# Kernel tuning notes

Hardware: AMD Instinct MI355X
Metric: run time of the kernel (lower is better)

The kernel has to match this reference:

```python
import jax, jax.numpy as jnp
import numpy as np

B, S, D, H = 2, 2048, 1024, 16
HD = D // H                      # 64
NUM_ROPE_DIMS = 2
NF = HD // (2 * NUM_ROPE_DIMS)   # 16 freqs per rope dim -> total HD//2
FFN_H = 4 * D


def householder_matrix(vs):
    """Product of Householder reflections: Q = prod_i (I - 2 v_i v_i^T / ||v_i||^2)."""
    dim = vs.shape[-1]
    def step(Q, v):
        v = v[:, None]
        Q = Q - (2.0 / (jnp.sum(v * v) + 1e-8)) * (v @ (v.T @ Q))
        return Q, None
    Q, _ = jax.lax.scan(step, jnp.eye(dim, dtype=vs.dtype), vs)
    return Q


def rmsnorm(x):
    # torch.nn.RMSNorm(eps=None) uses dtype eps, no affine
    return x * jax.lax.rsqrt(jnp.mean(x * x, axis=-1, keepdims=True) + jnp.finfo(x.dtype).eps)


def setup_inputs() -> dict:
    key = jax.random.key(0)
    ks = jax.random.split(key, 8)
    x = jax.random.normal(ks[0], (B, S, D), jnp.float32)
    mask = jnp.tril(jnp.ones((S, S), dtype=bool))          # causal block mask
    qkv_w = jax.random.normal(ks[1], (3 * D, D), jnp.float32) * 0.02
    out_w = jax.random.normal(ks[2], (D, D), jnp.float32) * 0.02
    gate_w = jax.random.normal(ks[3], (D, D), jnp.float32) * 0.02
    gate_b = jnp.zeros((D,), jnp.float32)
    w12 = jax.random.normal(ks[4], (2 * FFN_H, D), jnp.float32) * 0.02
    w3 = jax.random.normal(ks[5], (D, FFN_H), jnp.float32) * 0.02
    hh_vs = jax.random.normal(ks[6], (HD // 2, HD), jnp.float32) * 0.02
    inv_freq = 1.0 / (10000.0 ** (jnp.arange(NF, dtype=jnp.float32) / NF))
    pos = jnp.arange(S, dtype=jnp.float32)
    rope_pos = jnp.stack([pos, pos], axis=-1)              # [S, num_rope_dims]
    return dict(x=x, mask=mask, qkv_w=qkv_w, out_w=out_w, gate_w=gate_w,
                gate_b=gate_b, w12=w12, w3=w3, hh_vs=hh_vs,
                inv_freq=inv_freq, rope_pos=rope_pos)


def reference(x, mask, qkv_w, out_w, gate_w, gate_b, w12, w3, hh_vs, inv_freq, rope_pos):
    Bs, Ss, Ds = x.shape
    resid = x
    xn = rmsnorm(x)
    qkv = xn @ qkv_w.T                                      # [B,S,3D]
    q, k, v = jnp.split(qkv, 3, axis=-1)
    q = q.reshape(Bs, Ss, H, HD).transpose(0, 2, 1, 3)      # [B,H,S,HD]
    k = k.reshape(Bs, Ss, H, HD).transpose(0, 2, 1, 3)
    v = v.reshape(Bs, Ss, H, HD).transpose(0, 2, 1, 3)

    # RnRoPE: rotate into canonical basis, apply RoPE, rotate back
    Q = householder_matrix(hh_vs)                           # [HD,HD]
    q = q @ Q.T
    k = k @ Q.T
    # geo_state.scale = 1.0
    full = jnp.einsum('sd,f->sdf', rope_pos, inv_freq).reshape(Ss, -1)  # [S, HD//2]
    half = HD // 2
    full = full[:, :half]
    emb = jnp.concatenate([full, full], axis=-1)            # [S, HD]
    cos, sin = jnp.cos(emb), jnp.sin(emb)

    def rot(t):
        t1, t2 = jnp.split(t, 2, axis=-1)
        return t * cos + jnp.concatenate([-t2, t1], axis=-1) * sin

    q = rot(q) @ Q
    k = rot(k) @ Q

    # block-masked attention (flex_attention default scale = 1/sqrt(HD))
    scores = jnp.einsum('bhsd,bhtd->bhst', q, k) / jnp.sqrt(jnp.asarray(HD, x.dtype))
    scores = jnp.where(mask, scores, -jnp.inf)
    attn = jax.nn.softmax(scores, axis=-1)
    o = jnp.einsum('bhst,bhtd->bhsd', attn, v)
    o = o.transpose(0, 2, 1, 3).reshape(Bs, Ss, Ds)
    o = o @ out_w.T
    gate = jax.nn.sigmoid(o @ gate_w.T + gate_b)
    x = resid + o * gate

    # SwiGLU FFN
    resid2 = x
    xn2 = rmsnorm(x)
    x12 = xn2 @ w12.T
    x1, x2 = jnp.split(x12, 2, axis=-1)
    ffn = (jax.nn.silu(x1) * x2) @ w3.T
    return resid2 + ffn
```

## Files before the change

kernel.cpp:

```cpp
#include <hip/hip_runtime.h>
#include <hip/hip_bf16.h>
#include <math.h>

constexpr int Bc = 2, Sc = 2048, Dc = 1024, Hc = 16, HDc = 64;
constexpr int D3 = 3 * Dc;

typedef __bf16 bf16x8 __attribute__((ext_vector_type(8)));
typedef float f32x4 __attribute__((ext_vector_type(4)));

__device__ __forceinline__ void gll16(const void* g, void* l) {
  __builtin_amdgcn_global_load_lds((const __attribute__((address_space(1))) unsigned int*)g,
                                   (__attribute__((address_space(3))) unsigned int*)l,
                                   16, 0, 0);
}

__device__ __forceinline__ unsigned short f2bf(float v) {
  __hip_bfloat16 h = __float2bfloat16(v);
  return *(unsigned short*)&h;
}
__device__ __forceinline__ float b2f(unsigned short u) {
  unsigned v = ((unsigned)u) << 16;
  return __uint_as_float(v);
}

__global__ __launch_bounds__(256) void f2b_kernel(const float* __restrict__ in,
                                                  unsigned short* __restrict__ out) {
  int i = blockIdx.x * 256 + threadIdx.x;
  float4 v = ((const float4*)in)[i];
  ushort4 o;
  o.x = f2bf(v.x); o.y = f2bf(v.y); o.z = f2bf(v.z); o.w = f2bf(v.w);
  ((ushort4*)out)[i] = o;
}

__global__ __launch_bounds__(256) void rmsnorm_bf16_kernel(const float* __restrict__ in,
                                                           unsigned short* __restrict__ out) {
  int row = blockIdx.x;
  const float4* x4 = (const float4*)(in + (size_t)row * Dc);
  float4 v = x4[threadIdx.x];
  float s = v.x * v.x + v.y * v.y + v.z * v.z + v.w * v.w;
#pragma unroll
  for (int off = 1; off < 64; off <<= 1) s += __shfl_xor(s, off);
  __shared__ float wsum[4];
  if ((threadIdx.x & 63) == 0) wsum[threadIdx.x >> 6] = s;
  __syncthreads();
  float tot = wsum[0] + wsum[1] + wsum[2] + wsum[3];
  float r = rsqrtf(tot * (1.0f / Dc) + 1.1920928955078125e-07f);
  ushort4 o;
  o.x = f2bf(v.x * r); o.y = f2bf(v.y * r); o.z = f2bf(v.z * r); o.w = f2bf(v.w * r);
  ((ushort4*)(out + (size_t)row * Dc))[threadIdx.x] = o;
}

__global__ __launch_bounds__(64) void hh_kernel(const float* __restrict__ vs,
                                                float* __restrict__ Qout) {
  __shared__ float Qm[64][65];
  __shared__ float vsh[64];
  int t = threadIdx.x;
  for (int i = 0; i < 64; ++i) Qm[i][t] = (i == t) ? 1.0f : 0.0f;
  for (int it = 0; it < 32; ++it) {
    __syncthreads();
    vsh[t] = vs[it * 64 + t];
    __syncthreads();
    float nv = 0.0f;
    for (int i = 0; i < 64; ++i) nv += vsh[i] * vsh[i];
    float c = 2.0f / (nv + 1e-8f);
    float wj = 0.0f;
    for (int i = 0; i < 64; ++i) wj += vsh[i] * Qm[i][t];
    for (int i = 0; i < 64; ++i) Qm[i][t] -= c * vsh[i] * wj;
  }
  __syncthreads();
  for (int i = 0; i < 64; ++i) Qout[i * 64 + t] = Qm[i][t];
}

__global__ __launch_bounds__(256) void wqk_kernel(const float* __restrict__ W,
                                                  const float* __restrict__ Qm,
                                                  unsigned short* __restrict__ out) {
  int n = blockIdx.x;
  int r = n & 63;
  int base = n & ~63;
  int t = threadIdx.x;
  float a0 = 0, a1 = 0, a2 = 0, a3 = 0;
  const float4* Wp = (const float4*)(W + (size_t)base * 1024) + t;
#pragma unroll 8
  for (int e = 0; e < 64; ++e) {
    float q = Qm[r * 64 + e];
    float4 wv = Wp[(size_t)e * 256];
    a0 += q * wv.x; a1 += q * wv.y; a2 += q * wv.z; a3 += q * wv.w;
  }
  float sc = (n < 1024) ? 0.18033688f : 1.0f;
  ushort4 o;
  o.x = f2bf(a0 * sc); o.y = f2bf(a1 * sc); o.z = f2bf(a2 * sc); o.w = f2bf(a3 * sc);
  ((ushort4*)(out + (size_t)n * 1024))[t] = o;
}

__global__ __launch_bounds__(256) void rtab_kernel(const float* __restrict__ rope_pos,
                                                   const float* __restrict__ inv_freq,
                                                   float2* __restrict__ tab) {
  int id = blockIdx.x * 256 + threadIdx.x;
  int s = id >> 5, d = id & 31;
  float pos = rope_pos[s * 2 + (d >> 4)];
  float emb = pos * inv_freq[d & 15];
  tab[id] = make_float2(cosf(emb), sinf(emb));
}

__global__ __launch_bounds__(256) void rope_kernel(const unsigned short* __restrict__ qkv,
                                                   const float2* __restrict__ tab,
                                                   unsigned short* __restrict__ qb,
                                                   unsigned short* __restrict__ kb) {
  int t = threadIdx.x;
  int gid = blockIdx.x * 64 + (t >> 2);
  int sub = t & 3;
  int h = gid & 15;
  int which = (gid >> 4) & 1;
  int tok = gid >> 5;
  int s = tok & (Sc - 1), b = tok >> 11;
  const unsigned short* src = qkv + (size_t)tok * D3 + which * Dc + h * 64 + sub * 8;
  uint4 lov = *(const uint4*)src;
  uint4 hiv = *(const uint4*)(src + 32);
  const unsigned short* lp = (const unsigned short*)&lov;
  const unsigned short* hp = (const unsigned short*)&hiv;
  unsigned short olo[8], ohi[8];
  const float2* tp = tab + s * 32 + sub * 8;
#pragma unroll
  for (int i = 0; i < 8; ++i) {
    float2 cs = tp[i];
    float lo = b2f(lp[i]), hi = b2f(hp[i]);
    olo[i] = f2bf(lo * cs.x - hi * cs.y);
    ohi[i] = f2bf(hi * cs.x + lo * cs.y);
  }
  unsigned short* dst = (which ? kb : qb) + ((size_t)((b * Hc + h) * Sc + s)) * 64 + sub * 8;
  *(uint4*)dst = *(uint4*)olo;
  *(uint4*)(dst + 32) = *(uint4*)ohi;
}

__global__ __launch_bounds__(256) void vt_kernel(const unsigned short* __restrict__ qkv,
                                                 unsigned short* __restrict__ vtb) {
  __shared__ unsigned short tile[64 * 72];
  int st = blockIdx.x;
  int bh = blockIdx.y;
  int b = bh >> 4, h = bh & 15;
  int t = threadIdx.x;
  int srow = t >> 2, c16 = (t & 3) * 16;
  const unsigned short* src =
      qkv + (size_t)(b * Sc + st * 64 + srow) * D3 + 2 * Dc + h * 64 + c16;
  uint4 a0 = *(const uint4*)src;
  uint4 a1 = *(const uint4*)(src + 8);
  *(uint4*)(tile + srow * 72 + c16) = a0;
  *(uint4*)(tile + srow * 72 + c16 + 8) = a1;
  __syncthreads();
  int d = t >> 2, sch = (t & 3) * 16;
  unsigned short tmp[16];
#pragma unroll
  for (int i = 0; i < 16; ++i) tmp[i] = tile[(sch + i) * 72 + d];
  unsigned short* dst = vtb + ((size_t)(bh * 64 + d)) * Sc + st * 64 + sch;
  *(uint4*)dst = *(uint4*)tmp;
  *(uint4*)(dst + 8) = *(uint4*)(tmp + 8);
}

template <int MODE>
__global__ __launch_bounds__(256, 2) void mgemm(const unsigned short* __restrict__ A,
                                                const unsigned short* __restrict__ W,
                                                const unsigned short* __restrict__ W2,
                                                void* __restrict__ Cout,
                                                int M, int N, int K) {
  __shared__ unsigned short As[4096];
  __shared__ unsigned short Bs[4096];
  __shared__ unsigned short B2s[(MODE == 1) ? 4096 : 8];
  const int t = threadIdx.x;
  const int lane = t & 63;
  const int wave = t >> 6;
  const int wr = wave >> 1, wc = wave & 1;
  const int m0 = blockIdx.y * 128, n0 = blockIdx.x * 128;
  f32x4 acc[4][4] = {};
  f32x4 acc2[4][4] = {};
  const int srow = t >> 2;
  const int sch = (t & 3) * 8;
  const unsigned short* Ag = A + (size_t)(m0 + srow) * K + sch;
  const unsigned short* Wg = W + (size_t)(n0 + srow) * K + sch;
  const unsigned short* W2g = (MODE == 1) ? (W2 + (size_t)(n0 + srow) * K + sch) : nullptr;
  const size_t rstep = (size_t)64 * K;
  const int frow = lane & 15;
  const int fk = (lane >> 4) * 8;
  for (int k0 = 0; k0 < K; k0 += 32) {
    __syncthreads();
    gll16(Ag + k0, As + t * 8);
    gll16(Ag + k0 + rstep, As + 2048 + t * 8);
    gll16(Wg + k0, Bs + t * 8);
    gll16(Wg + k0 + rstep, Bs + 2048 + t * 8);
    if (MODE == 1) {
      gll16(W2g + k0, B2s + t * 8);
      gll16(W2g + k0 + rstep, B2s + 2048 + t * 8);
    }
    __syncthreads();
    bf16x8 af[4], bq[4];
#pragma unroll
    for (int i = 0; i < 4; ++i)
      af[i] = *(const bf16x8*)(As + (wr * 64 + i * 16 + frow) * 32 + fk);
#pragma unroll
    for (int j = 0; j < 4; ++j)
      bq[j] = *(const bf16x8*)(Bs + (wc * 64 + j * 16 + frow) * 32 + fk);
#pragma unroll
    for (int i = 0; i < 4; ++i)
#pragma unroll
      for (int j = 0; j < 4; ++j)
        acc[i][j] = __builtin_amdgcn_mfma_f32_16x16x32_bf16(af[i], bq[j], acc[i][j], 0, 0, 0);
    if (MODE == 1) {
#pragma unroll
      for (int j = 0; j < 4; ++j)
        bq[j] = *(const bf16x8*)(B2s + (wc * 64 + j * 16 + frow) * 32 + fk);
#pragma unroll
      for (int i = 0; i < 4; ++i)
#pragma unroll
        for (int j = 0; j < 4; ++j)
          acc2[i][j] = __builtin_amdgcn_mfma_f32_16x16x32_bf16(af[i], bq[j], acc2[i][j], 0, 0, 0);
    }
  }
  const int crow = wr * 64 + (lane >> 4) * 4;
  const int ccol = wc * 64 + (lane & 15);
#pragma unroll
  for (int i = 0; i < 4; ++i) {
#pragma unroll
    for (int j = 0; j < 4; ++j) {
#pragma unroll
      for (int r = 0; r < 4; ++r) {
        int row = m0 + crow + i * 16 + r;
        int col = n0 + ccol + j * 16;
        float v = acc[i][j][r];
        size_t off = (size_t)row * N + col;
        if (MODE == 1) {
          float sv = v / (1.0f + expf(-v));
          ((unsigned short*)Cout)[off] = f2bf(sv * acc2[i][j][r]);
        } else {
          ((unsigned short*)Cout)[off] = f2bf(v);
        }
      }
    }
  }
}

template <int MODE>
__global__ __launch_bounds__(256, 3) void mgemm64(const unsigned short* __restrict__ A,
                                                  const unsigned short* __restrict__ W,
                                                  const float* __restrict__ R,
                                                  const float* __restrict__ R2,
                                                  const float* __restrict__ bias,
                                                  void* __restrict__ Cout,
                                                  void* __restrict__ Cout2,
                                                  int M, int N, int K) {
  __shared__ unsigned short As[2048];
  __shared__ unsigned short Bs[4096];
  const int t = threadIdx.x;
  const int lane = t & 63;
  const int wave = t >> 6;
  const int wr = wave >> 1, wc = wave & 1;
  const int m0 = blockIdx.y * 64, n0 = blockIdx.x * 128;
  f32x4 acc[2][4] = {};
  const int srow = t >> 2;
  const int sch = (t & 3) * 8;
  const unsigned short* Ag = A + (size_t)(m0 + srow) * K + sch;
  const unsigned short* Wg = W + (size_t)(n0 + srow) * K + sch;
  const size_t rstep = (size_t)64 * K;
  const int frow = lane & 15;
  const int fk = (lane >> 4) * 8;
  for (int k0 = 0; k0 < K; k0 += 32) {
    __syncthreads();
    gll16(Ag + k0, As + t * 8);
    gll16(Wg + k0, Bs + t * 8);
    gll16(Wg + k0 + rstep, Bs + 2048 + t * 8);
    __syncthreads();
    bf16x8 af[2], bq[4];
#pragma unroll
    for (int i = 0; i < 2; ++i)
      af[i] = *(const bf16x8*)(As + (wr * 32 + i * 16 + frow) * 32 + fk);
#pragma unroll
    for (int j = 0; j < 4; ++j)
      bq[j] = *(const bf16x8*)(Bs + (wc * 64 + j * 16 + frow) * 32 + fk);
#pragma unroll
    for (int i = 0; i < 2; ++i)
#pragma unroll
      for (int j = 0; j < 4; ++j)
        acc[i][j] = __builtin_amdgcn_mfma_f32_16x16x32_bf16(af[i], bq[j], acc[i][j], 0, 0, 0);
  }
  const int crow = wr * 32 + (lane >> 4) * 4;
  const int ccol = wc * 64 + (lane & 15);
#pragma unroll
  for (int i = 0; i < 2; ++i) {
#pragma unroll
    for (int j = 0; j < 4; ++j) {
#pragma unroll
      for (int r = 0; r < 4; ++r) {
        int row = m0 + crow + i * 16 + r;
        int col = n0 + ccol + j * 16;
        float v = acc[i][j][r];
        size_t off = (size_t)row * N + col;
        if (MODE == 2) {
          ((float*)Cout)[off] = v + R[off];
        } else if (MODE == 4) {
          ((float*)Cout)[off] = v;
          ((unsigned short*)Cout2)[off] = f2bf(v);
        } else {
          float g = v + bias[col];
          float sg = 1.0f / (1.0f + expf(-g));
          ((float*)Cout)[off] = R[off] + R2[off] * sg;
        }
      }
    }
  }
}

__global__ __launch_bounds__(256) void mattn(const unsigned short* __restrict__ qb,
                                             const unsigned short* __restrict__ kb,
                                             const unsigned short* __restrict__ vtb,
                                             unsigned short* __restrict__ out) {
  __shared__ unsigned short Qs[8192];
  __shared__ unsigned short Ks[4096];
  __shared__ unsigned short Vts[4096];
  __shared__ unsigned short Ps[4 * 16 * 72];
  const int qt = gridDim.x - 1 - blockIdx.x;
  const int bh = blockIdx.y;
  const int b = bh >> 4, h = bh & 15;
  const int t = threadIdx.x, lane = t & 63, w = t >> 6;
  const int l15 = lane & 15, l4 = lane >> 4;
  const unsigned short* qbase = qb + ((size_t)bh * Sc + qt * 128) * 64;
  const unsigned short* kbase = kb + (size_t)bh * Sc * 64;
  const unsigned short* vbase = vtb + (size_t)bh * 64 * Sc;
#pragma unroll
  for (int i = 0; i < 4; ++i) {
    int idx = t + i * 256;
    int r = idx >> 3;
    int cg = (idx & 7) ^ (r & 7);
    gll16(qbase + (size_t)r * 64 + cg * 8, Qs + idx * 8);
  }
  bf16x8 qf[2][2];
  f32x4 oacc[2][4] = {};
  float lrow[2][4] = {};
  unsigned short* pw = Ps + w * 16 * 72;
  const int ktmax = 2 * qt + 1;
  for (int kt = 0; kt <= ktmax; ++kt) {
    __syncthreads();
    {
      int r = t >> 3;
      int cg = (t & 7) ^ (r & 7);
      gll16(kbase + (size_t)(kt * 64 + r) * 64 + cg * 8, Ks + t * 8);
      gll16(kbase + (size_t)(kt * 64 + r + 32) * 64 + cg * 8, Ks + 2048 + t * 8);
      gll16(vbase + (size_t)r * Sc + kt * 64 + cg * 8, Vts + t * 8);
      gll16(vbase + (size_t)(r + 32) * Sc + kt * 64 + cg * 8, Vts + 2048 + t * 8);
    }
    __syncthreads();
    if (kt == 0) {
#pragma unroll
      for (int ch = 0; ch < 2; ++ch) {
        int qrow = ch * 64 + w * 16 + l15;
#pragma unroll
        for (int kc = 0; kc < 2; ++kc)
          qf[ch][kc] = *(const bf16x8*)(Qs + qrow * 64 + (((kc * 4 + l4) ^ (l15 & 7)) * 8));
      }
    }
    const bool actA = (kt <= 2 * qt);
    f32x4 sc[2][4] = {};
#pragma unroll
    for (int kc = 0; kc < 2; ++kc) {
      bf16x8 kf[4];
#pragma unroll
      for (int j = 0; j < 4; ++j)
        kf[j] = *(const bf16x8*)(Ks + (j * 16 + l15) * 64 + (((kc * 4 + l4) ^ (l15 & 7)) * 8));
      if (actA) {
#pragma unroll
        for (int j = 0; j < 4; ++j)
          sc[0][j] = __builtin_amdgcn_mfma_f32_16x16x32_bf16(qf[0][kc], kf[j], sc[0][j], 0, 0, 0);
      }
#pragma unroll
      for (int j = 0; j < 4; ++j)
        sc[1][j] = __builtin_amdgcn_mfma_f32_16x16x32_bf16(qf[1][kc], kf[j], sc[1][j], 0, 0, 0);
    }
    const int rl = w * 16 + l4 * 4;
    if (kt == 2 * qt) {
#pragma unroll
      for (int j = 0; j < 4; ++j)
#pragma unroll
        for (int r = 0; r < 4; ++r)
          if (j * 16 + l15 > rl + r) sc[0][j][r] = -INFINITY;
    }
    if (kt == ktmax) {
#pragma unroll
      for (int j = 0; j < 4; ++j)
#pragma unroll
        for (int r = 0; r < 4; ++r)
          if (j * 16 + l15 > rl + r) sc[1][j][r] = -INFINITY;
    }
    bf16x8 vf[2][4];
#pragma unroll
    for (int kc = 0; kc < 2; ++kc)
#pragma unroll
      for (int j = 0; j < 4; ++j)
        vf[kc][j] = *(const bf16x8*)(Vts + (j * 16 + l15) * 64 + (((kc * 4 + l4) ^ (l15 & 7)) * 8));
#pragma unroll
    for (int ch = 0; ch < 2; ++ch) {
      if (ch == 0 && !actA) continue;
#pragma unroll
      for (int j = 0; j < 4; ++j)
#pragma unroll
        for (int r = 0; r < 4; ++r) {
          float p = exp2f(sc[ch][j][r]);
          lrow[ch][r] += p;
          pw[(l4 * 4 + r) * 72 + j * 16 + l15] = f2bf(p);
        }
      __asm__ __volatile__("s_waitcnt lgkmcnt(0)" ::: "memory");
#pragma unroll
      for (int kc = 0; kc < 2; ++kc) {
        bf16x8 pf = *(const bf16x8*)(pw + l15 * 72 + kc * 32 + l4 * 8);
#pragma unroll
        for (int j = 0; j < 4; ++j)
          oacc[ch][j] = __builtin_amdgcn_mfma_f32_16x16x32_bf16(pf, vf[kc][j], oacc[ch][j], 0, 0, 0);
      }
    }
  }
#pragma unroll
  for (int ch = 0; ch < 2; ++ch) {
#pragma unroll
    for (int r = 0; r < 4; ++r) {
      float s = lrow[ch][r];
      s += __shfl_xor(s, 1);
      s += __shfl_xor(s, 2);
      s += __shfl_xor(s, 4);
      s += __shfl_xor(s, 8);
      float inv = 1.0f / s;
#pragma unroll
      for (int j = 0; j < 4; ++j) {
        int srow = qt * 128 + ch * 64 + w * 16 + l4 * 4 + r;
        out[((size_t)(b * Sc + srow)) * Dc + h * 64 + j * 16 + l15] =
            f2bf(oacc[ch][j][r] * inv);
      }
    }
  }
}

extern "C" void kernel_launch(void* const* d_in, const int* in_sizes, int n_in,
                              void* d_out, int out_size, void* d_ws, size_t ws_size,
                              hipStream_t stream) {
  const float* x        = (const float*)d_in[0];
  const float* qkv_w    = (const float*)d_in[2];
  const float* out_w    = (const float*)d_in[3];
  const float* gate_w   = (const float*)d_in[4];
  const float* gate_b   = (const float*)d_in[5];
  const float* w12      = (const float*)d_in[6];
  const float* w3       = (const float*)d_in[7];
  const float* hh_vs    = (const float*)d_in[8];
  const float* inv_freq = (const float*)d_in[9];
  const float* rope_pos = (const float*)d_in[10];
  char* ws = (char*)d_ws;
  unsigned short* woutb  = (unsigned short*)(ws + 0);
  float2*         rtab   = (float2*)(ws + 2097152);
  unsigned short* wqkvb  = (unsigned short*)(ws + 4194304);
  unsigned short* attnb  = (unsigned short*)(ws + 4194304);
  float*          xmid   = (float*)(ws + 0);
  unsigned short* slotB  = (unsigned short*)(ws + 16777216);
  float*          oproj  = (float*)(ws + 25165824);
  unsigned short* w12b   = (unsigned short*)(ws + 25165824);
  unsigned short* wgateb = (unsigned short*)(ws + 41943040);
  unsigned short* w3b    = (unsigned short*)(ws + 41943040);
  unsigned short* qkvb   = (unsigned short*)(ws + 58720256);
  unsigned short* hbufb  = (unsigned short*)(ws + 58720256);
  unsigned short* qb     = (unsigned short*)(ws + 83886080);
  unsigned short* oprojb = (unsigned short*)(ws + 83886080);
  unsigned short* kb     = (unsigned short*)(ws + 92274688);
  unsigned short* vtb    = (unsigned short*)(ws + 100663296);
  float*          Qb     = (float*)(ws + 109051904);
  float* outp = (float*)d_out;

  hh_kernel<<<1, 64, 0, stream>>>(hh_vs, Qb);
  rtab_kernel<<<256, 256, 0, stream>>>(rope_pos, inv_freq, rtab);
  wqk_kernel<<<2048, 256, 0, stream>>>(qkv_w, Qb, wqkvb);
  f2b_kernel<<<1024, 256, 0, stream>>>(qkv_w + 2048 * 1024,
                                       wqkvb + 2048 * 1024);
  f2b_kernel<<<1024, 256, 0, stream>>>(out_w, woutb);
  f2b_kernel<<<1024, 256, 0, stream>>>(gate_w, wgateb);
  rmsnorm_bf16_kernel<<<4096, 256, 0, stream>>>(x, slotB);
  mgemm<3><<<dim3(24, 32), 256, 0, stream>>>(slotB, wqkvb, nullptr, qkvb, 4096, 3072, 1024);
  rope_kernel<<<2048, 256, 0, stream>>>(qkvb, rtab, qb, kb);
  vt_kernel<<<dim3(32, 32), 256, 0, stream>>>(qkvb, vtb);
  mattn<<<dim3(16, 32), 256, 0, stream>>>(qb, kb, vtb, attnb);
  mgemm64<4><<<dim3(8, 64), 256, 0, stream>>>(attnb, woutb, nullptr, nullptr, nullptr,
                                              oproj, oprojb, 4096, 1024, 1024);
  mgemm64<5><<<dim3(8, 64), 256, 0, stream>>>(oprojb, wgateb, x, oproj, gate_b,
                                              xmid, nullptr, 4096, 1024, 1024);
  f2b_kernel<<<8192, 256, 0, stream>>>(w12, w12b);
  f2b_kernel<<<4096, 256, 0, stream>>>(w3, w3b);
  rmsnorm_bf16_kernel<<<4096, 256, 0, stream>>>(xmid, slotB);
  mgemm<1><<<dim3(32, 32), 256, 0, stream>>>(slotB, w12b, w12b + 4194304, hbufb,
                                             4096, 4096, 1024);
  mgemm64<2><<<dim3(8, 64), 256, 0, stream>>>(hbufb, w3b, xmid, nullptr, nullptr,
                                              outp, nullptr, 4096, 1024, 4096);
}
```

Measured before the change: 563.3 us.

## Replace QKV and W12 GEMMs with 256x256 double-buffered 8-wave kernel

Adds a new GEMM kernel with 256x256 tiles, 512 threads and 8 waves. It double-buffers K=64 tiles in 128KB of LDS, interleaves global_load_lds prefetch with MFMA phases under manual barriers and setprio, and remaps block ids with an XCD-style swizzle. The w12 conversion now interleaves gate and up rows in 16-row groups, so a single GEMM computes both halves and fuses SiLU*mul in the epilogue. Larger tiles give more data reuse but allow only one block per CU, which may leave CUs idle on the QKV grid (192 blocks).

```diff
diff --git a/kernel.cpp b/kernel.cpp
--- a/kernel.cpp
+++ b/kernel.cpp
@@ -22,6 +22,8 @@
   unsigned v = ((unsigned)u) << 16;
   return __uint_as_float(v);
 }
+
+#define SBAR() asm volatile("s_barrier" ::: "memory")
 
 __global__ __launch_bounds__(256) void f2b_kernel(const float* __restrict__ in,
                                                   unsigned short* __restrict__ out) {
@@ -30,6 +32,17 @@
   ushort4 o;
   o.x = f2bf(v.x); o.y = f2bf(v.y); o.z = f2bf(v.z); o.w = f2bf(v.w);
   ((ushort4*)out)[i] = o;
+}
+
+__global__ __launch_bounds__(256) void w12i_kernel(const float* __restrict__ in,
+                                                   unsigned short* __restrict__ out) {
+  int r = blockIdx.x;
+  int g = r >> 5, u = r & 31;
+  int src = ((u < 16) ? 0 : 4096) + g * 16 + (u & 15);
+  float4 v = ((const float4*)(in + (size_t)src * 1024))[threadIdx.x];
+  ushort4 o;
+  o.x = f2bf(v.x); o.y = f2bf(v.y); o.z = f2bf(v.z); o.w = f2bf(v.w);
+  ((ushort4*)(out + (size_t)r * 1024))[threadIdx.x] = o;
 }
 
 __global__ __launch_bounds__(256) void rmsnorm_bf16_kernel(const float* __restrict__ in,
@@ -157,83 +170,131 @@
 }
 
 template <int MODE>
-__global__ __launch_bounds__(256, 2) void mgemm(const unsigned short* __restrict__ A,
-                                                const unsigned short* __restrict__ W,
-                                                const unsigned short* __restrict__ W2,
-                                                void* __restrict__ Cout,
-                                                int M, int N, int K) {
-  __shared__ unsigned short As[4096];
-  __shared__ unsigned short Bs[4096];
-  __shared__ unsigned short B2s[(MODE == 1) ? 4096 : 8];
+__global__ __launch_bounds__(512, 1) void mgemm8p(const unsigned short* __restrict__ A,
+                                                  const unsigned short* __restrict__ B,
+                                                  unsigned short* __restrict__ C,
+                                                  int M, int N, int K) {
+  __shared__ unsigned short lds[65536];
   const int t = threadIdx.x;
   const int lane = t & 63;
   const int wave = t >> 6;
-  const int wr = wave >> 1, wc = wave & 1;
-  const int m0 = blockIdx.y * 128, n0 = blockIdx.x * 128;
-  f32x4 acc[4][4] = {};
-  f32x4 acc2[4][4] = {};
-  const int srow = t >> 2;
-  const int sch = (t & 3) * 8;
-  const unsigned short* Ag = A + (size_t)(m0 + srow) * K + sch;
-  const unsigned short* Wg = W + (size_t)(n0 + srow) * K + sch;
-  const unsigned short* W2g = (MODE == 1) ? (W2 + (size_t)(n0 + srow) * K + sch) : nullptr;
-  const size_t rstep = (size_t)64 * K;
-  const int frow = lane & 15;
-  const int fk = (lane >> 4) * 8;
-  for (int k0 = 0; k0 < K; k0 += 32) {
-    __syncthreads();
-    gll16(Ag + k0, As + t * 8);
-    gll16(Ag + k0 + rstep, As + 2048 + t * 8);
-    gll16(Wg + k0, Bs + t * 8);
-    gll16(Wg + k0 + rstep, Bs + 2048 + t * 8);
-    if (MODE == 1) {
-      gll16(W2g + k0, B2s + t * 8);
-      gll16(W2g + k0 + rstep, B2s + 2048 + t * 8);
-    }
-    __syncthreads();
-    bf16x8 af[4], bq[4];
-#pragma unroll
-    for (int i = 0; i < 4; ++i)
-      af[i] = *(const bf16x8*)(As + (wr * 64 + i * 16 + frow) * 32 + fk);
-#pragma unroll
-    for (int j = 0; j < 4; ++j)
-      bq[j] = *(const bf16x8*)(Bs + (wc * 64 + j * 16 + frow) * 32 + fk);
-#pragma unroll
-    for (int i = 0; i < 4; ++i)
-#pragma unroll
-      for (int j = 0; j < 4; ++j)
-        acc[i][j] = __builtin_amdgcn_mfma_f32_16x16x32_bf16(af[i], bq[j], acc[i][j], 0, 0, 0);
-    if (MODE == 1) {
-#pragma unroll
-      for (int j = 0; j < 4; ++j)
-        bq[j] = *(const bf16x8*)(B2s + (wc * 64 + j * 16 + frow) * 32 + fk);
-#pragma unroll
-      for (int i = 0; i < 4; ++i)
-#pragma unroll
-        for (int j = 0; j < 4; ++j)
-          acc2[i][j] = __builtin_amdgcn_mfma_f32_16x16x32_bf16(af[i], bq[j], acc2[i][j], 0, 0, 0);
-    }
-  }
-  const int crow = wr * 64 + (lane >> 4) * 4;
-  const int ccol = wc * 64 + (lane & 15);
-#pragma unroll
-  for (int i = 0; i < 4; ++i) {
-#pragma unroll
-    for (int j = 0; j < 4; ++j) {
-#pragma unroll
-      for (int r = 0; r < 4; ++r) {
-        int row = m0 + crow + i * 16 + r;
-        int col = n0 + ccol + j * 16;
-        float v = acc[i][j][r];
-        size_t off = (size_t)row * N + col;
-        if (MODE == 1) {
+  const int wr = wave >> 2, wc = wave & 3;
+  const int l15 = lane & 15, l4 = lane >> 4;
+  const int gx = gridDim.x;
+  const int nwg = gx * gridDim.y;
+  const int id = blockIdx.y * gx + blockIdx.x;
+  const int swz = (id & 7) * (nwg >> 3) + (id >> 3);
+  const int m0 = (swz / gx) * 256;
+  const int n0 = (swz % gx) * 256;
+  const int NT = K >> 6;
+  const unsigned short* ag0 = A + (size_t)(m0 + (t >> 2)) * K + (t & 3) * 8;
+  const unsigned short* ag1 = ag0 + (size_t)128 * K;
+  const unsigned short* bg0 = B + (size_t)(n0 + (t >> 2)) * K + (t & 3) * 8;
+  const unsigned short* bg1 = bg0 + (size_t)128 * K;
+  const int t8 = t * 8;
+  gll16(ag0, lds + t8);
+  gll16(ag1, lds + 4096 + t8);
+  gll16(bg0, lds + 32768 + t8);
+  gll16(bg1, lds + 32768 + 4096 + t8);
+  gll16(ag0 + 32, lds + 8192 + t8);
+  gll16(ag1 + 32, lds + 8192 + 4096 + t8);
+  gll16(bg0 + 32, lds + 32768 + 8192 + t8);
+  gll16(bg1 + 32, lds + 32768 + 8192 + 4096 + t8);
+  asm volatile("s_waitcnt vmcnt(4)" ::: "memory");
+  SBAR();
+  f32x4 acc[8][4] = {};
+  for (int kt = 0; kt < NT; ++kt) {
+    const int cur = (kt & 1) << 14;
+    const int nxt = cur ^ 16384;
+    const int kof = ((kt + 1 < NT) ? (kt + 1) : kt) << 6;
+    const unsigned short* Ap = lds + cur;
+    const unsigned short* Bp = lds + 32768 + cur;
+    bf16x8 a[8], b0, b1;
+#pragma unroll
+    for (int i = 0; i < 8; ++i)
+      a[i] = *(const bf16x8*)(Ap + (wr * 128 + i * 16 + l15) * 32 + l4 * 8);
+    b0 = *(const bf16x8*)(Bp + (wc * 64 + l15) * 32 + l4 * 8);
+    b1 = *(const bf16x8*)(Bp + (wc * 64 + 16 + l15) * 32 + l4 * 8);
+    gll16(ag0 + kof, lds + nxt + t8);
+    gll16(ag1 + kof, lds + nxt + 4096 + t8);
+    SBAR();
+    __builtin_amdgcn_s_setprio(1);
+#pragma unroll
+    for (int i = 0; i < 8; ++i) {
+      acc[i][0] = __builtin_amdgcn_mfma_f32_16x16x32_bf16(a[i], b0, acc[i][0], 0, 0, 0);
+      acc[i][1] = __builtin_amdgcn_mfma_f32_16x16x32_bf16(a[i], b1, acc[i][1], 0, 0, 0);
+    }
+    __builtin_amdgcn_s_setprio(0);
+    SBAR();
+    b0 = *(const bf16x8*)(Bp + (wc * 64 + 32 + l15) * 32 + l4 * 8);
+    b1 = *(const bf16x8*)(Bp + (wc * 64 + 48 + l15) * 32 + l4 * 8);
+    gll16(bg0 + kof, lds + 32768 + nxt + t8);
+    gll16(bg1 + kof, lds + 32768 + nxt + 4096 + t8);
+    asm volatile("s_waitcnt vmcnt(4)" ::: "memory");
+    SBAR();
+    __builtin_amdgcn_s_setprio(1);
+#pragma unroll
+    for (int i = 0; i < 8; ++i) {
+      acc[i][2] = __builtin_amdgcn_mfma_f32_16x16x32_bf16(a[i], b0, acc[i][2], 0, 0, 0);
+      acc[i][3] = __builtin_amdgcn_mfma_f32_16x16x32_bf16(a[i], b1, acc[i][3], 0, 0, 0);
+    }
+    __builtin_amdgcn_s_setprio(0);
+    SBAR();
+#pragma unroll
+    for (int i = 0; i < 8; ++i)
+      a[i] = *(const bf16x8*)(Ap + 8192 + (wr * 128 + i * 16 + l15) * 32 + l4 * 8);
+    b0 = *(const bf16x8*)(Bp + 8192 + (wc * 64 + l15) * 32 + l4 * 8);
+    b1 = *(const bf16x8*)(Bp + 8192 + (wc * 64 + 16 + l15) * 32 + l4 * 8);
+    gll16(ag0 + kof + 32, lds + nxt + 8192 + t8);
+    gll16(ag1 + kof + 32, lds + nxt + 8192 + 4096 + t8);
+    SBAR();
+    __builtin_amdgcn_s_setprio(1);
+#pragma unroll
+    for (int i = 0; i < 8; ++i) {
+      acc[i][0] = __builtin_amdgcn_mfma_f32_16x16x32_bf16(a[i], b0, acc[i][0], 0, 0, 0);
+      acc[i][1] = __builtin_amdgcn_mfma_f32_16x16x32_bf16(a[i], b1, acc[i][1], 0, 0, 0);
+    }
+    __builtin_amdgcn_s_setprio(0);
+    SBAR();
+    b0 = *(const bf16x8*)(Bp + 8192 + (wc * 64 + 32 + l15) * 32 + l4 * 8);
+    b1 = *(const bf16x8*)(Bp + 8192 + (wc * 64 + 48 + l15) * 32 + l4 * 8);
+    gll16(bg0 + kof + 32, lds + 32768 + nxt + 8192 + t8);
+    gll16(bg1 + kof + 32, lds + 32768 + nxt + 8192 + 4096 + t8);
+    asm volatile("s_waitcnt vmcnt(4)" ::: "memory");
+    SBAR();
+    __builtin_amdgcn_s_setprio(1);
+#pragma unroll
+    for (int i = 0; i < 8; ++i) {
+      acc[i][2] = __builtin_amdgcn_mfma_f32_16x16x32_bf16(a[i], b0, acc[i][2], 0, 0, 0);
+      acc[i][3] = __builtin_amdgcn_mfma_f32_16x16x32_bf16(a[i], b1, acc[i][3], 0, 0, 0);
+    }
+    __builtin_amdgcn_s_setprio(0);
+    SBAR();
+  }
+  asm volatile("s_waitcnt vmcnt(0)" ::: "memory");
+  const int r0 = m0 + wr * 128 + l4 * 4;
+  if (MODE == 0) {
+    const int c0 = n0 + wc * 64 + l15;
+#pragma unroll
+    for (int i = 0; i < 8; ++i)
+#pragma unroll
+      for (int j = 0; j < 4; ++j)
+#pragma unroll
+        for (int r = 0; r < 4; ++r)
+          C[(size_t)(r0 + i * 16 + r) * N + c0 + j * 16] = f2bf(acc[i][j][r]);
+  } else {
+    const int nc = N >> 1;
+    const int c0 = (n0 >> 1) + wc * 32 + l15;
+#pragma unroll
+    for (int i = 0; i < 8; ++i)
+#pragma unroll
+      for (int p = 0; p < 2; ++p)
+#pragma unroll
+        for (int r = 0; r < 4; ++r) {
+          float v = acc[i][2 * p][r];
           float sv = v / (1.0f + expf(-v));
-          ((unsigned short*)Cout)[off] = f2bf(sv * acc2[i][j][r]);
-        } else {
-          ((unsigned short*)Cout)[off] = f2bf(v);
+          C[(size_t)(r0 + i * 16 + r) * nc + c0 + p * 16] = f2bf(sv * acc[i][2 * p + 1][r]);
         }
-      }
-    }
   }
 }
 
@@ -475,7 +536,7 @@
   f2b_kernel<<<1024, 256, 0, stream>>>(out_w, woutb);
   f2b_kernel<<<1024, 256, 0, stream>>>(gate_w, wgateb);
   rmsnorm_bf16_kernel<<<4096, 256, 0, stream>>>(x, slotB);
-  mgemm<3><<<dim3(24, 32), 256, 0, stream>>>(slotB, wqkvb, nullptr, qkvb, 4096, 3072, 1024);
+  mgemm8p<0><<<dim3(12, 16), 512, 0, stream>>>(slotB, wqkvb, qkvb, 4096, 3072, 1024);
   rope_kernel<<<2048, 256, 0, stream>>>(qkvb, rtab, qb, kb);
   vt_kernel<<<dim3(32, 32), 256, 0, stream>>>(qkvb, vtb);
   mattn<<<dim3(16, 32), 256, 0, stream>>>(qb, kb, vtb, attnb);
@@ -483,11 +544,10 @@
                                               oproj, oprojb, 4096, 1024, 1024);
   mgemm64<5><<<dim3(8, 64), 256, 0, stream>>>(oprojb, wgateb, x, oproj, gate_b,
                                               xmid, nullptr, 4096, 1024, 1024);
-  f2b_kernel<<<8192, 256, 0, stream>>>(w12, w12b);
+  w12i_kernel<<<8192, 256, 0, stream>>>(w12, w12b);
   f2b_kernel<<<4096, 256, 0, stream>>>(w3, w3b);
   rmsnorm_bf16_kernel<<<4096, 256, 0, stream>>>(xmid, slotB);
-  mgemm<1><<<dim3(32, 32), 256, 0, stream>>>(slotB, w12b, w12b + 4194304, hbufb,
-                                             4096, 4096, 1024);
+  mgemm8p<1><<<dim3(32, 16), 512, 0, stream>>>(slotB, w12b, hbufb, 4096, 8192, 1024);
   mgemm64<2><<<dim3(8, 64), 256, 0, stream>>>(hbufb, w3b, xmid, nullptr, nullptr,
                                               outp, nullptr, 4096, 1024, 4096);
 }
```

Result: no change. 562.8 us (-0.1%).
